# Kernel tuning notes

Measured on AMD Instinct MI355X. Metric: run time of the kernel, lower is better.

The kernel has to match this reference:

```python
import jax, jax.numpy as jnp
import numpy as np

SX, SY, C, K = 256, 256, 3, 15
DD, DT, SIGMA = 5, 0.2, 0.65
C0 = tuple(i % C for i in range(K))
C1 = tuple(tuple(i for i in range(K) if i % C == c) for c in range(C))
MA = DD - SIGMA  # flow magnitude bound


def _sobel(A):
    # A: (X, Y, c) -> (X, Y, 2, c); matches jsp.signal.convolve2d(..., mode='same')
    kx = jnp.array([[1., 0., -1.], [2., 0., -2.], [1., 0., -1.]], dtype=A.dtype)
    ky = kx.T
    # convolve2d flips the kernel; emulate true convolution by correlating with rot180 kernels
    kern = jnp.stack([jnp.rot90(ky, 2), jnp.rot90(kx, 2)])[:, None]  # (2,1,3,3): [grad_y, grad_x]
    x = jnp.transpose(A, (2, 0, 1))[:, None]                          # (c,1,X,Y)
    out = jax.lax.conv_general_dilated(x, kern, (1, 1), 'SAME')       # (c,2,X,Y)
    return jnp.transpose(out, (2, 3, 1, 0))                           # (X,Y,2,c)


def _reintegration(A, P, F):
    # Reintegration tracking, has_hidden=True, border='wall', mix='softmax'
    xs, ys = jnp.meshgrid(jnp.arange(SX), jnp.arange(SY))
    pos = (jnp.dstack((ys, xs)) + .5).astype(A.dtype)     # (X,Y,2) cell centers (row, col)
    mus = pos[..., None] + jnp.clip(DT * F, -MA, MA)      # (X,Y,2,C) target centers
    mus = jnp.clip(mus, SIGMA, SX - SIGMA)                # wall border
    shifts = jnp.array([(dx, dy) for dx in range(-DD, DD + 1) for dy in range(-DD, DD + 1)])
    cap = min(1., 2 * SIGMA)

    def step(sft):
        sh = (sft[0], sft[1])
        Ar = jnp.roll(A, sh, axis=(0, 1))
        Pr = jnp.roll(P, sh, axis=(0, 1))
        mur = jnp.roll(mus, sh, axis=(0, 1))
        dpmu = jnp.abs(pos[..., None] - mur)              # (X,Y,2,C)
        sz = .5 - dpmu + SIGMA
        area = jnp.prod(jnp.clip(sz, 0., cap), axis=2) / (4 * SIGMA ** 2)  # (X,Y,C)
        return Ar * area, Pr

    nA, nP = jax.vmap(step)(shifts)                       # (N,X,Y,C), (N,X,Y,K)
    expnA = jnp.exp(nA.sum(-1, keepdims=True)) - 1.       # softmax mix rule
    newA = nA.sum(0)
    newP = (nP * expnA).sum(0) / (expnA.sum(0) + 1e-10)
    return newA, newP


def _forward(A, P, fK_real, fK_imag, m, s):
    fK = fK_real + 1j * fK_imag                           # (X,Y,K) kernel FFTs
    fA = jnp.fft.fft2(A, axes=(0, 1))                     # (X,Y,C)
    fAk = jnp.take(fA, jnp.array(C0), axis=2)             # (X,Y,K) per-kernel source channel
    U = jnp.real(jnp.fft.ifft2(fK * fAk, axes=(0, 1)))    # (X,Y,K)
    U = (2. * jnp.exp(-((U - m) ** 2) / (2. * s ** 2)) - 1.) * P  # growth(U,m,s)*P
    U = jnp.dstack([U[:, :, C1[c]].sum(-1) for c in range(C)])    # (X,Y,C)
    F = _sobel(U)                                         # (X,Y,2,C)
    Cg = _sobel(A.sum(-1, keepdims=True))                 # (X,Y,2,1)
    alpha = jnp.clip((A[:, :, None, :] / 2.) ** 2, 0., 1.)
    F = jnp.clip(F * (1. - alpha) - Cg * alpha, -MA, MA)
    return _reintegration(A, P, F)


def setup_inputs() -> dict:
    key = jax.random.key(0)
    kA, kP, kr, km, ks, ka, kb, kw = jax.random.split(key, 8)
    A = jax.random.uniform(kA, (SX, SY, C), dtype=jnp.float32)
    P = jax.random.uniform(kP, (SX, SY, K), dtype=jnp.float32)
    R = 15.0
    r = jax.random.uniform(kr, (K,), minval=.2, maxval=1.)
    m = jax.random.uniform(km, (K,), minval=.05, maxval=.5, dtype=jnp.float32)
    s = jax.random.uniform(ks, (K,), minval=.001, maxval=.18, dtype=jnp.float32)
    a = jax.random.uniform(ka, (K, 3))
    b = jax.random.uniform(kb, (K, 3), minval=.001, maxval=1.)
    w = jax.random.uniform(kw, (K, 3), minval=.01, maxval=.5)
    mid = SX // 2
    D = jnp.linalg.norm(jnp.mgrid[-mid:mid, -mid:mid], axis=0)[..., None] / ((R + 15.) * r)  # (X,Y,K)
    Kk = jax.nn.sigmoid(-(D - 1.) * 10.) * (b * jnp.exp(-((D[..., None] - a) / w) ** 2)).sum(-1)
    nK = Kk / Kk.sum((0, 1), keepdims=True)
    fK = jnp.fft.fft2(jnp.fft.fftshift(nK, axes=(0, 1)), axes=(0, 1))
    return {"A": A, "P": P,
            "fK_real": jnp.real(fK).astype(jnp.float32),
            "fK_imag": jnp.imag(fK).astype(jnp.float32),
            "m": m, "s": s}


def reference(A, P, fK_real, fK_imag, m, s):
    return _forward(A, P, fK_real, fK_imag, m, s)
```

## Files before the change

kernel.cpp:

```cpp
#include <hip/hip_runtime.h>


#define XY  65536
#define NC  3
#define NK  15
#define WPAD 260

__device__ __forceinline__ float2 cmul(float2 a, float2 b) {
  return make_float2(a.x * b.x - a.y * b.y, a.x * b.y + a.y * b.x);
}

__device__ __forceinline__ int swz(int i) { return i ^ ((i >> 4) & 15); }

__device__ __forceinline__ void wave_fence() {
  asm volatile("" ::: "memory");
  __builtin_amdgcn_wave_barrier();
  asm volatile("" ::: "memory");
}

__device__ __forceinline__ void fft256_wave(float2* b0, float2* b1, int t, float sign) {
  float2* src = b0;
  float2* dst = b1;
#pragma unroll
  for (int stage = 0; stage < 4; ++stage) {
    wave_fence();
    const int Ns = 1 << (2 * stage);
    float2 v0 = src[swz(t)];
    float2 v1 = src[swz(t + 64)];
    float2 v2 = src[swz(t + 128)];
    float2 v3 = src[swz(t + 192)];
    const int jm = t & (Ns - 1);
    float ang = sign * 6.283185307179586f * (float)jm / (float)(Ns * 4);
    float sn, cs;
    __sincosf(ang, &sn, &cs);
    float2 w1 = make_float2(cs, sn);
    float2 w2 = cmul(w1, w1);
    float2 w3 = cmul(w2, w1);
    v1 = cmul(v1, w1);
    v2 = cmul(v2, w2);
    v3 = cmul(v3, w3);
    float2 a0 = make_float2(v0.x + v2.x, v0.y + v2.y);
    float2 a1 = make_float2(v0.x - v2.x, v0.y - v2.y);
    float2 a2 = make_float2(v1.x + v3.x, v1.y + v3.y);
    float2 a3 = make_float2(v1.x - v3.x, v1.y - v3.y);
    float2 ia3 = make_float2(-sign * a3.y, sign * a3.x);
    const int idxD = ((t >> (2 * stage)) << (2 * stage)) * 4 + jm;
    dst[swz(idxD)]          = make_float2(a0.x + a2.x, a0.y + a2.y);
    dst[swz(idxD + Ns)]     = make_float2(a1.x + ia3.x, a1.y + ia3.y);
    dst[swz(idxD + 2 * Ns)] = make_float2(a0.x - a2.x, a0.y - a2.y);
    dst[swz(idxD + 3 * Ns)] = make_float2(a1.x - ia3.x, a1.y - ia3.y);
    float2* tmp = src; src = dst; dst = tmp;
  }
  wave_fence();
}

__global__ __launch_bounds__(64) void k_rowfft(const float* __restrict__ A,
                                               float2* __restrict__ RF) {
  __shared__ float2 b0[256], b1[256];
  const int t = threadIdx.x;
  const int x = blockIdx.x & 255;
  const int c = blockIdx.x >> 8;
#pragma unroll
  for (int r = 0; r < 4; ++r) {
    int y = t + 64 * r;
    b0[swz(y)] = make_float2(A[(x * 256 + y) * NC + c], 0.0f);
  }
  fft256_wave(b0, b1, t, -1.0f);
#pragma unroll
  for (int r = 0; r < 4; ++r) {
    int y = t + 64 * r;
    RF[(c * 256 + x) * 256 + y] = b0[swz(y)];
  }
}

__global__ __launch_bounds__(512, 1) void k_colfft(const float* __restrict__ fKr,
                                                   const float* __restrict__ fKi,
                                                   const float2* __restrict__ RF,
                                                   float2* __restrict__ T2) {
  __shared__ float2 lds0[8 * WPAD];
  __shared__ float2 lds1[8 * WPAD];
  const int tid = threadIdx.x;
  const int k = blockIdx.x >> 5;
  const int y0 = (blockIdx.x & 31) << 3;
  const int c = k % 3;
  const int w = tid >> 6, lane = tid & 63;
  const int y = y0 + w;

  float2 Kv[4];
#pragma unroll
  for (int r = 0; r < 4; ++r) {
    const int xx = lane + 64 * r;
    const int fi = (xx * 256 + y) * NK + k;
    Kv[r] = make_float2(fKr[fi], fKi[fi]);
  }

  {
    const int q = tid & 3;
#pragma unroll
    for (int r = 0; r < 2; ++r) {
      const int x = (tid >> 2) + (r << 7);
      const float4* src = (const float4*)(RF + (c * XY + x * 256 + y0));
      float4 v = src[q];
      lds0[(2 * q) * WPAD + swz(x)]     = make_float2(v.x, v.y);
      lds0[(2 * q + 1) * WPAD + swz(x)] = make_float2(v.z, v.w);
    }
  }
  __syncthreads();

  float2* b0 = lds0 + w * WPAD;
  float2* b1 = lds1 + w * WPAD;
  fft256_wave(b0, b1, lane, -1.0f);

  float2 fa[4];
#pragma unroll
  for (int r = 0; r < 4; ++r) fa[r] = b0[swz(lane + 64 * r)];
#pragma unroll
  for (int r = 0; r < 4; ++r) {
    const int x = lane + 64 * r;
    b0[swz(x)] = cmul(Kv[r], fa[r]);
  }
  fft256_wave(b0, b1, lane, 1.0f);
  __syncthreads();

  {
    const int q = tid & 3;
#pragma unroll
    for (int r = 0; r < 2; ++r) {
      const int x = (tid >> 2) + (r << 7);
      float2 v0 = lds0[(2 * q) * WPAD + swz(x)];
      float2 v1 = lds0[(2 * q + 1) * WPAD + swz(x)];
      float4* dst = (float4*)(T2 + (k * XY + x * 256 + y0));
      dst[q] = make_float4(v0.x, v0.y, v1.x, v1.y);
    }
  }
}

__global__ __launch_bounds__(320, 1) void k_irowfft_growth(const float2* __restrict__ T2,
                                                           const float* __restrict__ P,
                                                           const float* __restrict__ m,
                                                           const float* __restrict__ s,
                                                           float* __restrict__ Ucol) {
  __shared__ float2 lds0[5 * WPAD];
  __shared__ float2 lds1[5 * WPAD];
  __shared__ float accs[5 * WPAD];
  const int tid = threadIdx.x;
  const int x = blockIdx.x & 255;
  const int c = blockIdx.x >> 8;
  const int j = tid >> 6, lane = tid & 63;
  const int k = c + 3 * j;

  float pv[4];
#pragma unroll
  for (int r = 0; r < 4; ++r) {
    int y = lane + 64 * r;
    pv[r] = P[(x * 256 + y) * NK + k];
  }
  const float mk = m[k];
  const float sk = s[k];
  const float inv2s2 = 0.5f / (sk * sk);

  float2* b0 = lds0 + j * WPAD;
  float2* b1 = lds1 + j * WPAD;
  const float2* src = T2 + (k * XY + x * 256);
#pragma unroll
  for (int r = 0; r < 4; ++r) {
    int y = lane + 64 * r;
    b0[swz(y)] = src[y];
  }
  fft256_wave(b0, b1, lane, 1.0f);

#pragma unroll
  for (int r = 0; r < 4; ++r) {
    int y = lane + 64 * r;
    float U = b0[swz(y)].x * (1.0f / 65536.0f);
    float d = U - mk;
    float g = 2.0f * __expf(-d * d * inv2s2) - 1.0f;
    accs[j * WPAD + y] = g * pv[r];
  }
  __syncthreads();
  if (tid < 256) {
    float sum = 0.f;
#pragma unroll
    for (int j2 = 0; j2 < 5; ++j2) sum += accs[j2 * WPAD + tid];
    Ucol[c * XY + x * 256 + tid] = sum;
  }
}

__global__ __launch_bounds__(256) void k_flow(const float* __restrict__ A,
                                              const float* __restrict__ Ucol,
                                              float* __restrict__ F) {
  const int idx = blockIdx.x * 256 + threadIdx.x;
  const int x = idx >> 8;
  const int y = idx & 255;
  const float MA = 4.35f;

  float u[3][3][3];
  float asum[3][3];
#pragma unroll
  for (int di = -1; di <= 1; ++di) {
#pragma unroll
    for (int dj = -1; dj <= 1; ++dj) {
      int xi = x + di, yj = y + dj;
      bool inb = ((unsigned)xi < 256u) && ((unsigned)yj < 256u);
      float a0 = 0.f, a1 = 0.f, a2 = 0.f, as = 0.f;
      if (inb) {
        int b = xi * 256 + yj;
        a0 = Ucol[0 * XY + b];
        a1 = Ucol[1 * XY + b];
        a2 = Ucol[2 * XY + b];
        const float* ap = A + b * NC;
        as = ap[0] + ap[1] + ap[2];
      }
      u[0][di + 1][dj + 1] = a0;
      u[1][di + 1][dj + 1] = a1;
      u[2][di + 1][dj + 1] = a2;
      asum[di + 1][dj + 1] = as;
    }
  }
  float cg0 = (asum[2][0] + 2.f * asum[2][1] + asum[2][2]) -
              (asum[0][0] + 2.f * asum[0][1] + asum[0][2]);
  float cg1 = (asum[0][2] + 2.f * asum[1][2] + asum[2][2]) -
              (asum[0][0] + 2.f * asum[1][0] + asum[2][0]);
  const int b = x * 256 + y;
#pragma unroll
  for (int c = 0; c < NC; ++c) {
    float f0 = (u[c][2][0] + 2.f * u[c][2][1] + u[c][2][2]) -
               (u[c][0][0] + 2.f * u[c][0][1] + u[c][0][2]);
    float f1 = (u[c][0][2] + 2.f * u[c][1][2] + u[c][2][2]) -
               (u[c][0][0] + 2.f * u[c][1][0] + u[c][2][0]);
    float ah = A[b * NC + c] * 0.5f;
    float al = fminf(ah * ah, 1.0f);
    f0 = fminf(fmaxf(f0 * (1.f - al) - cg0 * al, -MA), MA);
    f1 = fminf(fmaxf(f1 * (1.f - al) - cg1 * al, -MA), MA);
    F[(b * 2 + 0) * NC + c] = f0;
    F[(b * 2 + 1) * NC + c] = f1;
  }
}

__global__ __launch_bounds__(256) void k_reint(const float* __restrict__ A,
                                               const float* __restrict__ P,
                                               const float* __restrict__ F,
                                               float* __restrict__ outA,
                                               float* __restrict__ outP) {
  __shared__ float4 lA[400];
  __shared__ float4 lF[2][400];
  __shared__ float4 lP[4][400];
  const int tid = threadIdx.x;
  const int x0 = (blockIdx.x >> 4) << 4;
  const int y0 = (blockIdx.x & 15) << 4;

  for (int cell = tid; cell < 400; cell += 256) {
    const int r = cell / 20, cc = cell - r * 20;
    const int sx = (x0 + r - 2) & 255;
    const int sy = (y0 + cc - 2) & 255;
    const int sb = sx * 256 + sy;
    const float* ap = A + sb * NC;
    lA[cell] = make_float4(ap[0], ap[1], ap[2], 0.f);
    const float* fp = F + sb * 6;
    lF[0][cell] = make_float4(fp[0], fp[1], fp[2], fp[3]);
    lF[1][cell] = make_float4(fp[4], fp[5], 0.f, 0.f);
    const float* pp = P + sb * NK;
    lP[0][cell] = make_float4(pp[0], pp[1], pp[2], pp[3]);
    lP[1][cell] = make_float4(pp[4], pp[5], pp[6], pp[7]);
    lP[2][cell] = make_float4(pp[8], pp[9], pp[10], pp[11]);
    lP[3][cell] = make_float4(pp[12], pp[13], pp[14], 0.f);
  }
  __syncthreads();

  const int lx = tid >> 4, ly = tid & 15;
  const int x = x0 + lx, y = y0 + ly;
  const float SIGMA = 0.65f;
  const float INV4S2 = 1.0f / (4.0f * 0.65f * 0.65f);
  const float DT = 0.2f;
  const float px = x + 0.5f;
  const float py = y + 0.5f;

  float accA0 = 0.f, accA1 = 0.f, accA2 = 0.f;
  float accP[15];
#pragma unroll
  for (int k = 0; k < NK; ++k) accP[k] = 0.f;
  float esum = 0.f;

#pragma unroll
  for (int dx = -2; dx <= 2; ++dx) {
#pragma unroll
    for (int dy = -2; dy <= 2; ++dy) {
      const int lc = (lx + 2 - dx) * 20 + (ly + 2 - dy);
      const int sx = (x - dx) & 255;
      const int sy = (y - dy) & 255;
      const float spx = sx + 0.5f;
      const float spy = sy + 0.5f;
      const float4 av = lA[lc];
      const float4 fv0 = lF[0][lc];
      const float4 fv1 = lF[1][lc];
      float mu0 = fminf(fmaxf(spx + DT * fv0.x, SIGMA), 256.f - SIGMA);
      float mu1 = fminf(fmaxf(spy + DT * fv0.w, SIGMA), 256.f - SIGMA);
      float sz0 = fminf(fmaxf(0.5f - fabsf(px - mu0) + SIGMA, 0.f), 1.f);
      float sz1 = fminf(fmaxf(0.5f - fabsf(py - mu1) + SIGMA, 0.f), 1.f);
      float na0 = av.x * (sz0 * sz1 * INV4S2);
      mu0 = fminf(fmaxf(spx + DT * fv0.y, SIGMA), 256.f - SIGMA);
      mu1 = fminf(fmaxf(spy + DT * fv1.x, SIGMA), 256.f - SIGMA);
      sz0 = fminf(fmaxf(0.5f - fabsf(px - mu0) + SIGMA, 0.f), 1.f);
      sz1 = fminf(fmaxf(0.5f - fabsf(py - mu1) + SIGMA, 0.f), 1.f);
      float na1 = av.y * (sz0 * sz1 * INV4S2);
      mu0 = fminf(fmaxf(spx + DT * fv0.z, SIGMA), 256.f - SIGMA);
      mu1 = fminf(fmaxf(spy + DT * fv1.y, SIGMA), 256.f - SIGMA);
      sz0 = fminf(fmaxf(0.5f - fabsf(px - mu0) + SIGMA, 0.f), 1.f);
      sz1 = fminf(fmaxf(0.5f - fabsf(py - mu1) + SIGMA, 0.f), 1.f);
      float na2 = av.z * (sz0 * sz1 * INV4S2);

      const float e = __expf(na0 + na1 + na2) - 1.0f;
      accA0 += na0; accA1 += na1; accA2 += na2;
      esum += e;
      const float4 p0 = lP[0][lc];
      const float4 p1 = lP[1][lc];
      const float4 p2 = lP[2][lc];
      const float4 p3 = lP[3][lc];
      accP[0]  += p0.x * e; accP[1]  += p0.y * e; accP[2]  += p0.z * e; accP[3]  += p0.w * e;
      accP[4]  += p1.x * e; accP[5]  += p1.y * e; accP[6]  += p1.z * e; accP[7]  += p1.w * e;
      accP[8]  += p2.x * e; accP[9]  += p2.y * e; accP[10] += p2.z * e; accP[11] += p2.w * e;
      accP[12] += p3.x * e; accP[13] += p3.y * e; accP[14] += p3.z * e;
    }
  }

  const int b = x * 256 + y;
  outA[b * NC + 0] = accA0;
  outA[b * NC + 1] = accA1;
  outA[b * NC + 2] = accA2;
  const float inv = 1.0f / (esum + 1e-10f);
#pragma unroll
  for (int k = 0; k < NK; ++k) outP[b * NK + k] = accP[k] * inv;
}

extern "C" void kernel_launch(void* const* d_in, const int* in_sizes, int n_in,
                              void* d_out, int out_size, void* d_ws, size_t ws_size,
                              hipStream_t stream) {
  const float* A   = (const float*)d_in[0];
  const float* P   = (const float*)d_in[1];
  const float* fKr = (const float*)d_in[2];
  const float* fKi = (const float*)d_in[3];
  const float* m   = (const float*)d_in[4];
  const float* s   = (const float*)d_in[5];

  float* ws = (float*)d_ws;
  float2* RF   = (float2*)ws;
  float2* T2   = RF + NC * XY;
  float*  Ucol = (float*)(T2 + NK * XY);
  float*  F    = Ucol + NC * XY;

  float* outA = (float*)d_out;
  float* outP = outA + NC * XY;

  k_rowfft<<<NC * 256, 64, 0, stream>>>(A, RF);
  k_colfft<<<NK * 32, 512, 0, stream>>>(fKr, fKi, RF, T2);
  k_irowfft_growth<<<NC * 256, 320, 0, stream>>>(T2, P, m, s, Ucol);
  k_flow<<<256, 256, 0, stream>>>(A, Ucol, F);
  k_reint<<<256, 256, 0, stream>>>(A, P, F, outA, outP);
}
```

Baseline: 105.5 us.

## Fuse flow computation into reintegration kernel and batch row FFTs per block

Merges the flow (Sobel gradient) kernel into the reintegration kernel. Each 16x16 tile loads a 22x22 halo of A and U into LDS and computes F for its 20x20 halo on-chip, so the global F buffer and one launch go away. This recomputes the flow on halo cells redundantly and adds a second barrier and extra LDS. Separately, the row FFT now runs four waves per 256-thread block instead of one wave per 64-thread block, cutting the block count by four.

```diff
diff --git a/kernel.cpp b/kernel.cpp
--- a/kernel.cpp
+++ b/kernel.cpp
@@ -54,21 +54,24 @@
   wave_fence();
 }
 
-__global__ __launch_bounds__(64) void k_rowfft(const float* __restrict__ A,
-                                               float2* __restrict__ RF) {
-  __shared__ float2 b0[256], b1[256];
-  const int t = threadIdx.x;
-  const int x = blockIdx.x & 255;
-  const int c = blockIdx.x >> 8;
-#pragma unroll
-  for (int r = 0; r < 4; ++r) {
-    int y = t + 64 * r;
+__global__ __launch_bounds__(256) void k_rowfft(const float* __restrict__ A,
+                                                float2* __restrict__ RF) {
+  __shared__ float2 l0[4 * WPAD], l1[4 * WPAD];
+  const int tid = threadIdx.x;
+  const int w = tid >> 6, lane = tid & 63;
+  const int c = blockIdx.x >> 6;
+  const int x = ((blockIdx.x & 63) << 2) + w;
+  float2* b0 = l0 + w * WPAD;
+  float2* b1 = l1 + w * WPAD;
+#pragma unroll
+  for (int r = 0; r < 4; ++r) {
+    int y = lane + 64 * r;
     b0[swz(y)] = make_float2(A[(x * 256 + y) * NC + c], 0.0f);
   }
-  fft256_wave(b0, b1, t, -1.0f);
-#pragma unroll
-  for (int r = 0; r < 4; ++r) {
-    int y = t + 64 * r;
+  fft256_wave(b0, b1, lane, -1.0f);
+#pragma unroll
+  for (int r = 0; r < 4; ++r) {
+    int y = lane + 64 * r;
     RF[(c * 256 + x) * 256 + y] = b0[swz(y)];
   }
 }
@@ -186,80 +189,38 @@
   }
 }
 
-__global__ __launch_bounds__(256) void k_flow(const float* __restrict__ A,
-                                              const float* __restrict__ Ucol,
-                                              float* __restrict__ F) {
-  const int idx = blockIdx.x * 256 + threadIdx.x;
-  const int x = idx >> 8;
-  const int y = idx & 255;
-  const float MA = 4.35f;
-
-  float u[3][3][3];
-  float asum[3][3];
-#pragma unroll
-  for (int di = -1; di <= 1; ++di) {
-#pragma unroll
-    for (int dj = -1; dj <= 1; ++dj) {
-      int xi = x + di, yj = y + dj;
-      bool inb = ((unsigned)xi < 256u) && ((unsigned)yj < 256u);
-      float a0 = 0.f, a1 = 0.f, a2 = 0.f, as = 0.f;
-      if (inb) {
-        int b = xi * 256 + yj;
-        a0 = Ucol[0 * XY + b];
-        a1 = Ucol[1 * XY + b];
-        a2 = Ucol[2 * XY + b];
-        const float* ap = A + b * NC;
-        as = ap[0] + ap[1] + ap[2];
-      }
-      u[0][di + 1][dj + 1] = a0;
-      u[1][di + 1][dj + 1] = a1;
-      u[2][di + 1][dj + 1] = a2;
-      asum[di + 1][dj + 1] = as;
-    }
-  }
-  float cg0 = (asum[2][0] + 2.f * asum[2][1] + asum[2][2]) -
-              (asum[0][0] + 2.f * asum[0][1] + asum[0][2]);
-  float cg1 = (asum[0][2] + 2.f * asum[1][2] + asum[2][2]) -
-              (asum[0][0] + 2.f * asum[1][0] + asum[2][0]);
-  const int b = x * 256 + y;
-#pragma unroll
-  for (int c = 0; c < NC; ++c) {
-    float f0 = (u[c][2][0] + 2.f * u[c][2][1] + u[c][2][2]) -
-               (u[c][0][0] + 2.f * u[c][0][1] + u[c][0][2]);
-    float f1 = (u[c][0][2] + 2.f * u[c][1][2] + u[c][2][2]) -
-               (u[c][0][0] + 2.f * u[c][1][0] + u[c][2][0]);
-    float ah = A[b * NC + c] * 0.5f;
-    float al = fminf(ah * ah, 1.0f);
-    f0 = fminf(fmaxf(f0 * (1.f - al) - cg0 * al, -MA), MA);
-    f1 = fminf(fmaxf(f1 * (1.f - al) - cg1 * al, -MA), MA);
-    F[(b * 2 + 0) * NC + c] = f0;
-    F[(b * 2 + 1) * NC + c] = f1;
-  }
-}
-
-__global__ __launch_bounds__(256) void k_reint(const float* __restrict__ A,
-                                               const float* __restrict__ P,
-                                               const float* __restrict__ F,
-                                               float* __restrict__ outA,
-                                               float* __restrict__ outP) {
-  __shared__ float4 lA[400];
+__global__ __launch_bounds__(256) void k_flow_reint(const float* __restrict__ A,
+                                                    const float* __restrict__ P,
+                                                    const float* __restrict__ Ucol,
+                                                    float* __restrict__ outA,
+                                                    float* __restrict__ outP) {
+  __shared__ float4 lAF[484];
+  __shared__ float4 lU[484];
   __shared__ float4 lF[2][400];
   __shared__ float4 lP[4][400];
   const int tid = threadIdx.x;
   const int x0 = (blockIdx.x >> 4) << 4;
   const int y0 = (blockIdx.x & 15) << 4;
-
+  const float MA = 4.35f;
+  const float SIGMA = 0.65f;
+  const float INV4S2 = 1.0f / (4.0f * 0.65f * 0.65f);
+  const float DT = 0.2f;
+
+  for (int cell = tid; cell < 484; cell += 256) {
+    const int r = cell / 22, cc = cell - r * 22;
+    const int sx = (x0 + r - 3) & 255;
+    const int sy = (y0 + cc - 3) & 255;
+    const int sb = sx * 256 + sy;
+    const float* ap = A + sb * NC;
+    const float a0 = ap[0], a1 = ap[1], a2 = ap[2];
+    lAF[cell] = make_float4(a0, a1, a2, a0 + a1 + a2);
+    lU[cell] = make_float4(Ucol[sb], Ucol[XY + sb], Ucol[2 * XY + sb], 0.f);
+  }
   for (int cell = tid; cell < 400; cell += 256) {
     const int r = cell / 20, cc = cell - r * 20;
     const int sx = (x0 + r - 2) & 255;
     const int sy = (y0 + cc - 2) & 255;
-    const int sb = sx * 256 + sy;
-    const float* ap = A + sb * NC;
-    lA[cell] = make_float4(ap[0], ap[1], ap[2], 0.f);
-    const float* fp = F + sb * 6;
-    lF[0][cell] = make_float4(fp[0], fp[1], fp[2], fp[3]);
-    lF[1][cell] = make_float4(fp[4], fp[5], 0.f, 0.f);
-    const float* pp = P + sb * NK;
+    const float* pp = P + (sx * 256 + sy) * NK;
     lP[0][cell] = make_float4(pp[0], pp[1], pp[2], pp[3]);
     lP[1][cell] = make_float4(pp[4], pp[5], pp[6], pp[7]);
     lP[2][cell] = make_float4(pp[8], pp[9], pp[10], pp[11]);
@@ -267,11 +228,56 @@
   }
   __syncthreads();
 
+  for (int cell = tid; cell < 400; cell += 256) {
+    const int fr = cell / 20, fc = cell - fr * 20;
+    const int sx = (x0 + fr - 2) & 255;
+    const int sy = (y0 + fc - 2) & 255;
+    float u[3][3][3];
+    float as[3][3];
+#pragma unroll
+    for (int di = -1; di <= 1; ++di) {
+#pragma unroll
+      for (int dj = -1; dj <= 1; ++dj) {
+        const bool zb = (sx == 0 && di < 0) || (sx == 255 && di > 0) ||
+                        (sy == 0 && dj < 0) || (sy == 255 && dj > 0);
+        float4 uv = make_float4(0.f, 0.f, 0.f, 0.f);
+        float av = 0.f;
+        if (!zb) {
+          const int lc = (fr + 1 + di) * 22 + (fc + 1 + dj);
+          uv = lU[lc];
+          av = lAF[lc].w;
+        }
+        u[0][di + 1][dj + 1] = uv.x;
+        u[1][di + 1][dj + 1] = uv.y;
+        u[2][di + 1][dj + 1] = uv.z;
+        as[di + 1][dj + 1] = av;
+      }
+    }
+    const float cg0 = (as[2][0] + 2.f * as[2][1] + as[2][2]) -
+                      (as[0][0] + 2.f * as[0][1] + as[0][2]);
+    const float cg1 = (as[0][2] + 2.f * as[1][2] + as[2][2]) -
+                      (as[0][0] + 2.f * as[1][0] + as[2][0]);
+    const float4 ac = lAF[(fr + 1) * 22 + (fc + 1)];
+    float fo[2][3];
+#pragma unroll
+    for (int c = 0; c < NC; ++c) {
+      float f0 = (u[c][2][0] + 2.f * u[c][2][1] + u[c][2][2]) -
+                 (u[c][0][0] + 2.f * u[c][0][1] + u[c][0][2]);
+      float f1 = (u[c][0][2] + 2.f * u[c][1][2] + u[c][2][2]) -
+                 (u[c][0][0] + 2.f * u[c][1][0] + u[c][2][0]);
+      const float a = (c == 0) ? ac.x : (c == 1) ? ac.y : ac.z;
+      const float ah = a * 0.5f;
+      const float al = fminf(ah * ah, 1.0f);
+      fo[0][c] = fminf(fmaxf(f0 * (1.f - al) - cg0 * al, -MA), MA);
+      fo[1][c] = fminf(fmaxf(f1 * (1.f - al) - cg1 * al, -MA), MA);
+    }
+    lF[0][cell] = make_float4(fo[0][0], fo[0][1], fo[0][2], fo[1][0]);
+    lF[1][cell] = make_float4(fo[1][1], fo[1][2], 0.f, 0.f);
+  }
+  __syncthreads();
+
   const int lx = tid >> 4, ly = tid & 15;
   const int x = x0 + lx, y = y0 + ly;
-  const float SIGMA = 0.65f;
-  const float INV4S2 = 1.0f / (4.0f * 0.65f * 0.65f);
-  const float DT = 0.2f;
   const float px = x + 0.5f;
   const float py = y + 0.5f;
 
@@ -286,11 +292,12 @@
 #pragma unroll
     for (int dy = -2; dy <= 2; ++dy) {
       const int lc = (lx + 2 - dx) * 20 + (ly + 2 - dy);
+      const int la = (lx + 3 - dx) * 22 + (ly + 3 - dy);
       const int sx = (x - dx) & 255;
       const int sy = (y - dy) & 255;
       const float spx = sx + 0.5f;
       const float spy = sy + 0.5f;
-      const float4 av = lA[lc];
+      const float4 av = lAF[la];
       const float4 fv0 = lF[0][lc];
       const float4 fv1 = lF[1][lc];
       float mu0 = fminf(fmaxf(spx + DT * fv0.x, SIGMA), 256.f - SIGMA);
@@ -346,14 +353,12 @@
   float2* RF   = (float2*)ws;
   float2* T2   = RF + NC * XY;
   float*  Ucol = (float*)(T2 + NK * XY);
-  float*  F    = Ucol + NC * XY;
 
   float* outA = (float*)d_out;
   float* outP = outA + NC * XY;
 
-  k_rowfft<<<NC * 256, 64, 0, stream>>>(A, RF);
+  k_rowfft<<<NC * 64, 256, 0, stream>>>(A, RF);
   k_colfft<<<NK * 32, 512, 0, stream>>>(fKr, fKi, RF, T2);
   k_irowfft_growth<<<NC * 256, 320, 0, stream>>>(T2, P, m, s, Ucol);
-  k_flow<<<256, 256, 0, stream>>>(A, Ucol, F);
-  k_reint<<<256, 256, 0, stream>>>(A, P, F, outA, outP);
-}
+  k_flow_reint<<<256, 256, 0, stream>>>(A, P, Ucol, outA, outP);
+}
```

New measurement: 103.2 us. 2.2% less time.
